# Optimization experiments

Hardware: AMD Instinct MI355X
Metric: run time of the kernel (lower is better)

The kernel has to match this reference:

```python
import jax, jax.numpy as jnp
import numpy as np

N_NODES = 20000
N_EDGES = 100000
NODE_IN = 4
EDGE_IN = 4
HIDDEN = 64
N_GRAPHS = 64
LN_EPS = 1e-5


def _glorot(key, shape):
    fan_in, fan_out = shape[0], shape[1]
    lim = jnp.sqrt(6.0 / (fan_in + fan_out))
    return jax.random.uniform(key, shape, jnp.float32, -lim, lim)


def setup_inputs() -> dict:
    key = jax.random.key(0)
    ks = jax.random.split(key, 24)
    inp = {
        "x": jax.random.normal(ks[0], (N_NODES, NODE_IN), jnp.float32),
        "edge_index": jax.random.randint(ks[1], (2, N_EDGES), 0, N_NODES),
        "edge_attr": jax.random.normal(ks[2], (N_EDGES, EDGE_IN), jnp.float32),
        "batch": jnp.sort(jax.random.randint(ks[3], (N_NODES,), 0, N_GRAPHS)),
        # layer 1: edge MLP edge_in->64->node_in*hidden, root lin, bias, LN
        "eW1_1": _glorot(ks[4], (EDGE_IN, 64)),
        "eb1_1": jnp.zeros((64,), jnp.float32),
        "eW2_1": _glorot(ks[5], (64, NODE_IN * HIDDEN)),
        "eb2_1": jnp.zeros((NODE_IN * HIDDEN,), jnp.float32),
        "root1": _glorot(ks[6], (NODE_IN, HIDDEN)),
        "bias1": jnp.zeros((HIDDEN,), jnp.float32),
        "g1": jnp.ones((HIDDEN,), jnp.float32),
        "b1": jnp.zeros((HIDDEN,), jnp.float32),
        # layer 2: edge MLP edge_in->128->hidden*hidden, root lin, bias, LN
        "eW1_2": _glorot(ks[7], (EDGE_IN, 128)),
        "eb1_2": jnp.zeros((128,), jnp.float32),
        "eW2_2": _glorot(ks[8], (128, HIDDEN * HIDDEN)),
        "eb2_2": jnp.zeros((HIDDEN * HIDDEN,), jnp.float32),
        "root2": _glorot(ks[9], (HIDDEN, HIDDEN)),
        "bias2": jnp.zeros((HIDDEN,), jnp.float32),
        "g2": jnp.ones((HIDDEN,), jnp.float32),
        "b2": jnpp_zeros if False else jnp.zeros((HIDDEN,), jnp.float32),
    }
    return inp


def _nnconv(h, src, dst, edge_attr, eW1, eb1, eW2, eb2, root, bias, in_ch, out_ch):
    # per-edge weight matrix from edge MLP: [E, in_ch, out_ch]
    ew = jnp.maximum(edge_attr @ eW1 + eb1, 0.0) @ eW2 + eb2
    ew = ew.reshape(-1, in_ch, out_ch)
    # gather src features, per-edge small matmul
    msg = jnp.einsum("ei,eio->eo", h[src], ew)  # [E, out_ch]
    # scatter-mean to dst
    agg = jax.ops.segment_sum(msg, dst, num_segments=N_NODES)
    deg = jax.ops.segment_sum(jnp.ones((msg.shape[0],), msg.dtype), dst, num_segments=N_NODES)
    agg = agg / jnp.maximum(deg, 1.0)[:, None]
    return agg + h @ root + bias


def _layernorm(v, g, b):
    mu = jnp.mean(v, axis=-1, keepdims=True)
    var = jnp.mean((v - mu) ** 2, axis=-1, keepdims=True)
    return (v - mu) * jax.lax.rsqrt(var + LN_EPS) * g + b


def reference(x, edge_index, edge_attr, batch,
              eW1_1, eb1_1, eW2_1, eb2_1, root1, bias1, g1, b1,
              eW1_2, eb1_2, eW2_2, eb2_2, root2, bias2, g2, b2):
    src, dst = edge_index[0], edge_index[1]
    h = _nnconv(x, src, dst, edge_attr, eW1_1, eb1_1, eW2_1, eb2_1, root1, bias1, NODE_IN, HIDDEN)
    h = _layernorm(jnp.maximum(h, 0.0), g1, b1)  # dropout is identity in eval
    h = _nnconv(h, src, dst, edge_attr, eW1_2, eb1_2, eW2_2, eb2_2, root2, bias2, HIDDEN, HIDDEN)
    h = _layernorm(jnp.maximum(h, 0.0), g2, b2)
    # global mean pool over graphs
    num = jax.ops.segment_sum(h, batch, num_segments=N_GRAPHS)
    cnt = jax.ops.segment_sum(jnp.ones((h.shape[0],), h.dtype), batch, num_segments=N_GRAPHS)
    return num / jnp.maximum(cnt, 1.0)[:, None]
```

## Files before the change

### kernel.cpp

```cpp
#include <hip/hip_runtime.h>
#include <hip/hip_bf16.h>
#include <hip/hip_fp16.h>

#define NN 20000
#define NE 100000
#define NGR 64
#define NGRP 1250

using bf16 = __hip_bfloat16;
typedef __attribute__((ext_vector_type(8))) short v8s;
typedef __attribute__((ext_vector_type(4))) float v4f;
typedef _Float16 h2f __attribute__((ext_vector_type(2)));

__device__ __forceinline__ float ldf(const void* p, int idx, int isbf) {
  if (isbf) return __bfloat162float(((const bf16*)p)[idx]);
  return ((const float*)p)[idx];
}
__device__ __forceinline__ unsigned short f2bfbits(float v) {
  unsigned int b = __float_as_uint(v);
  b += 0x7fffu + ((b >> 16) & 1u);
  return (unsigned short)(b >> 16);
}

__device__ __forceinline__ unsigned int pkh2(float a, float b) {
#if __has_builtin(__builtin_amdgcn_cvt_pkrtz)
  auto r = __builtin_amdgcn_cvt_pkrtz(a, b);
  return __builtin_bit_cast(unsigned int, r);
#else
  unsigned int lo = __half_as_ushort(__float2half(a));
  unsigned int hi = __half_as_ushort(__float2half(b));
  return lo | (hi << 16);
#endif
}
__device__ __forceinline__ float dot2a(unsigned int z, unsigned int q, float c) {
#if __has_builtin(__builtin_amdgcn_fdot2)
  return __builtin_amdgcn_fdot2(__builtin_bit_cast(h2f, z),
                                __builtin_bit_cast(h2f, q), c, false);
#else
  h2f zh = __builtin_bit_cast(h2f, z), qh = __builtin_bit_cast(h2f, q);
  return c + (float)zh.x * (float)qh.x + (float)zh.y * (float)qh.y;
#endif
}

__global__ __launch_bounds__(64) void k_detect(const unsigned short* __restrict__ xr,
                                               int* __restrict__ flag) {
  const int t = threadIdx.x;
  int cnt = 0;
#pragma unroll
  for (int j = 0; j < 4; j++) {
    unsigned short w = xr[t * 4 + j];
    int ex = (w >> 7) & 0xFF;
    cnt += (ex >= 118 && ex <= 131) ? 1 : 0;
  }
#pragma unroll
  for (int m = 32; m >= 1; m >>= 1) cnt += __shfl_xor(cnt, m, 64);
  if (t == 0) *flag = (cnt >= 192) ? 1 : 0;
}

__global__ __launch_bounds__(256) void k_deg(const int* __restrict__ ei,
                                             int* __restrict__ deg_src,
                                             int* __restrict__ deg_in) {
  int e = blockIdx.x * 256 + threadIdx.x;
  if (e < NE) {
    atomicAdd(&deg_src[ei[e]], 1);
    atomicAdd(&deg_in[ei[NE + e]], 1);
  }
}

__global__ __launch_bounds__(256) void k_scan(const int* __restrict__ deg,
                                              int* __restrict__ off,
                                              int* __restrict__ cur) {
  constexpr int T = 256, CH = 80;
  __shared__ int sums[T];
  const int t = threadIdx.x;
  const int base = t * CH;
  int s = 0;
  for (int j = 0; j < CH; j++) {
    int i = base + j;
    s += (i < NN) ? deg[i] : 0;
  }
  sums[t] = s;
  __syncthreads();
  for (int st = 1; st < T; st <<= 1) {
    int v = (t >= st) ? sums[t - st] : 0;
    __syncthreads();
    sums[t] += v;
    __syncthreads();
  }
  int run = sums[t] - s;
  for (int j = 0; j < CH; j++) {
    int i = base + j;
    if (i < NN) {
      int v = deg[i];
      off[i] = run;
      cur[i] = run;
      run += v;
    }
  }
  if (t == T - 1) off[NN] = sums[T - 1];
}

__global__ __launch_bounds__(256) void k_scatter(const int* __restrict__ ei,
                                                 int* __restrict__ cur,
                                                 int* __restrict__ ebs) {
  int e = blockIdx.x * 256 + threadIdx.x;
  if (e < NE) {
    int p = atomicAdd(&cur[ei[e]], 1);
    if (p >= 0 && p < NE) ebs[p] = e;
  }
}

template <int KH, int IN>
__global__ __launch_bounds__(256) void k_shuffle(const void* __restrict__ W2,
                                                 unsigned short* __restrict__ W2s,
                                                 const int* __restrict__ flag) {
  const int f = *flag;
  int t = blockIdx.x * 256 + threadIdx.x;
  int lane = t & 63, F = t >> 6;
  int ks = F & 1, ot = (F >> 1) & 3, k2 = F >> 3;
  int quad = lane >> 4, col = lane & 15;
  unsigned short tmp[8];
#pragma unroll
  for (int j = 0; j < 8; j++) {
    int i = ks * 32 + quad * 8 + j;
    tmp[j] = f2bfbits(ldf(W2, k2 * (IN * 64) + i * 64 + ot * 16 + col, f));
  }
  *(uint4*)(W2s + (size_t)F * 512 + lane * 8) = *(uint4*)tmp;
}

template <int IN, int KH, int HMODE, int QMFMA, int CSPLIT>
__global__ __launch_bounds__(512, 4) void k_fused2(
    const void* __restrict__ h_in, const void* __restrict__ eW1,
    const void* __restrict__ eb1, const void* __restrict__ W2,
    const unsigned short* __restrict__ W2s, const void* __restrict__ eb2,
    const void* __restrict__ ea, const int* __restrict__ ei,
    const int* __restrict__ src_off, const int* __restrict__ ebs,
    float* __restrict__ agg, const int* __restrict__ flag) {
  constexpr int NPG = 16, KC = 16, NCH = KH / KC, NCHL = NCH / CSPLIT, EB = 128;
  constexpr int QNS = (KC / 2) * 64 + 4;
  constexpr int ZROW = 10;

  __shared__ float hA[NPG][IN];
  __shared__ _Float16 r2h[NPG][64];
  __shared__ __align__(16) unsigned int Qc[NPG * QNS];
  __shared__ float eW1S[4][KH];
  __shared__ float ebS[KH];
  __shared__ float eaS[EB][4];
  __shared__ __align__(16) unsigned int zB[EB * ZROW];
  __shared__ int esrcS[EB], edstS[EB];
  __shared__ __align__(16) unsigned short hF[QMFMA ? 2 : 1][64][8];

  const int f = *flag;
  const int tid = threadIdx.x;
  const int o = tid & 63;
  const int kq = tid >> 6;
  const int g = blockIdx.y;
  const int n0 = blockIdx.x * NPG;

  for (int idx = tid; idx < NPG * IN; idx += 512) {
    int n = idx / IN, i = idx - n * IN;
    hA[n][i] = (HMODE == 1) ? ((const float*)h_in)[(n0 + n) * IN + i]
                            : ldf(h_in, (n0 + n) * IN + i, f);
  }
  for (int idx = tid; idx < 4 * KH; idx += 512)
    ((float*)eW1S)[idx] = ldf(eW1, idx, f);
  for (int idx = tid; idx < KH; idx += 512) ebS[idx] = ldf(eb1, idx, f);
  __syncthreads();

  if (g == 0) {
    const int nb = kq * 2;
    float a0 = 0.f, a1 = 0.f;
    for (int i = 0; i < IN; i++) {
      float wv = ldf(eb2, i * 64 + o, f);
      a0 += hA[nb + 0][i] * wv;
      a1 += hA[nb + 1][i] * wv;
    }
    r2h[nb + 0][o] = (_Float16)a0;
    r2h[nb + 1][o] = (_Float16)a1;
  }
  if constexpr (QMFMA) {
    if (tid < 128) {
      int l = tid & 63, ks = tid >> 6;
#pragma unroll
      for (int j = 0; j < 8; j++)
        hF[ks][l][j] = f2bfbits(hA[l & 15][ks * 32 + (l >> 4) * 8 + j]);
    }
  }
  __syncthreads();

  v8s aF0 = {}, aF1 = {};
  if constexpr (QMFMA) {
    aF0 = *(const v8s*)&hF[0][o][0];
    aF1 = *(const v8s*)&hF[1][o][0];
  }

  const int estart = src_off[n0];
  const int ecount = src_off[n0 + NPG] - estart;

  for (int b = 0; b < ecount; b += EB) {
    const int bc = min(EB, ecount - b);
    __syncthreads();
    if (tid < bc) {
      int eid = ebs[estart + b + tid];
      esrcS[tid] = ei[eid] - n0;
      edstS[tid] = ei[NE + eid];
#pragma unroll
      for (int i = 0; i < 4; i++) eaS[tid][i] = ldf(ea, eid * 4 + i, f);
    }
    __syncthreads();

    float msg[EB / 8];
#pragma unroll
    for (int j = 0; j < EB / 8; j++) msg[j] = 0.f;
    const int lo = (bc * kq) >> 3, hi = (bc * (kq + 1)) >> 3;

    for (int cl = 0; cl < NCHL; cl++) {
      const int c = g * NCHL + cl;
      v4f acc8[8];
      float accv[NPG * 2];
      if constexpr (QMFMA) {
#pragma unroll
        for (int nt = 0; nt < 8; nt++) {
          acc8[nt] = (v4f){0.f, 0.f, 0.f, 0.f};
          const int k2 = c * KC + kq * 2 + (nt >> 2);
          const int Fb = (k2 * 4 + (nt & 3)) * 2;
          v8s b0 = *(const v8s*)(W2s + (size_t)Fb * 512 + o * 8);
          v8s b1 = *(const v8s*)(W2s + (size_t)(Fb + 1) * 512 + o * 8);
          acc8[nt] =
              __builtin_amdgcn_mfma_f32_16x16x32_bf16(aF0, b0, acc8[nt], 0, 0, 0);
          acc8[nt] =
              __builtin_amdgcn_mfma_f32_16x16x32_bf16(aF1, b1, acc8[nt], 0, 0, 0);
        }
      } else {
        const int kg0 = c * KC + kq * 2;
        const int w2base = kg0 * (IN * 64) + o;
        float w0[IN], w1[IN];
#pragma unroll
        for (int j = 0; j < IN; j++) {
          w0[j] = ldf(W2, w2base + j * 64, f);
          w1[j] = ldf(W2, w2base + IN * 64 + j * 64, f);
        }
#pragma unroll
        for (int n = 0; n < NPG; n++) {
          float a0 = 0.f, a1 = 0.f;
#pragma unroll
          for (int j = 0; j < IN; j++) {
            float hv = hA[n][j];
            a0 += hv * w0[j];
            a1 += hv * w1[j];
          }
          accv[n * 2 + 0] = a0;
          accv[n * 2 + 1] = a1;
        }
      }
      const int ze = tid & 127, kseg = tid >> 7;
      float zv[4];
      if (ze < bc) {
#pragma unroll
        for (int jj = 0; jj < 4; jj++) {
          int k2 = c * KC + kseg * 4 + jj;
          float a = ebS[k2];
#pragma unroll
          for (int i = 0; i < 4; i++) a += eaS[ze][i] * eW1S[i][k2];
          zv[jj] = fmaxf(a, 0.f);
        }
      }
      __syncthreads();
      if constexpr (QMFMA) {
        const int quad = o >> 4;
#pragma unroll
        for (int nt = 0; nt < 4; nt++) {
          const int o2 = nt * 16 + (o & 15);
#pragma unroll
          for (int r = 0; r < 4; r++)
            Qc[(quad * 4 + r) * QNS + kq * 64 + o2] =
                pkh2(acc8[nt][r], acc8[nt + 4][r]);
        }
      } else {
#pragma unroll
        for (int n = 0; n < NPG; n++)
          Qc[n * QNS + kq * 64 + o] = pkh2(accv[n * 2 + 0], accv[n * 2 + 1]);
      }
      if (ze < bc) {
        uint2 p;
        p.x = pkh2(zv[0], zv[1]);
        p.y = pkh2(zv[2], zv[3]);
        *(uint2*)&zB[ze * ZROW + kseg * 2] = p;
      }
      __syncthreads();
      unsigned int q0 = 0, q1 = 0, q2 = 0, q3 = 0, q4 = 0, q5 = 0, q6 = 0,
                   q7 = 0;
      int sprev = -1;
#pragma unroll
      for (int j = 0; j < EB / 8; j++) {
        const int e = lo + j;
        if (e < hi) {
          const int s = esrcS[e];
          if (s != sprev) {
            const unsigned int* qp = &Qc[s * QNS + o];
            q0 = qp[0 * 64]; q1 = qp[1 * 64]; q2 = qp[2 * 64]; q3 = qp[3 * 64];
            q4 = qp[4 * 64]; q5 = qp[5 * 64]; q6 = qp[6 * 64]; q7 = qp[7 * 64];
            sprev = s;
          }
          const uint2 za = *(const uint2*)&zB[e * ZROW + 0];
          const uint2 zb2 = *(const uint2*)&zB[e * ZROW + 2];
          const uint2 zc = *(const uint2*)&zB[e * ZROW + 4];
          const uint2 zd = *(const uint2*)&zB[e * ZROW + 6];
          float m = msg[j];
          m = dot2a(za.x, q0, m);
          m = dot2a(za.y, q1, m);
          m = dot2a(zb2.x, q2, m);
          m = dot2a(zb2.y, q3, m);
          m = dot2a(zc.x, q4, m);
          m = dot2a(zc.y, q5, m);
          m = dot2a(zd.x, q6, m);
          m = dot2a(zd.y, q7, m);
          msg[j] = m;
        }
      }
    }
#pragma unroll
    for (int j = 0; j < EB / 8; j++) {
      const int e = lo + j;
      if (e < hi) {
        float add = msg[j];
        if (g == 0) add += (float)r2h[esrcS[e]][o];
        atomicAdd(&agg[(size_t)edstS[e] * 64 + o], add);
      }
    }
  }
}

__device__ __forceinline__ float wave_sum(float v) {
#pragma unroll
  for (int m = 32; m >= 1; m >>= 1) v += __shfl_xor(v, m, 64);
  return v;
}

__global__ __launch_bounds__(256, 4) void k_node1(
    const float* __restrict__ agg1, const int* __restrict__ deg_in,
    const void* __restrict__ x, const void* __restrict__ root1,
    const void* __restrict__ bias1, const void* __restrict__ g1,
    const void* __restrict__ b1, float* __restrict__ h1,
    const int* __restrict__ flag) {
  constexpr int NPW = 8;
  const int f = *flag;
  const int tid = threadIdx.x;
  const int o = tid & 63;
  const int w = tid >> 6;
  float r1c[4];
#pragma unroll
  for (int i = 0; i < 4; i++) r1c[i] = ldf(root1, i * 64 + o, f);
  const float bs = ldf(bias1, o, f);
  const float gv = ldf(g1, o, f);
  const float bv = ldf(b1, o, f);
  const int wid = blockIdx.x * 4 + w;
  const int nbeg = wid * NPW;
  const int nend = min(nbeg + NPW, NN);
  for (int n = nbeg; n < nend; n++) {
    float v = agg1[(size_t)n * 64 + o] / fmaxf((float)deg_in[n], 1.f) + bs;
#pragma unroll
    for (int i = 0; i < 4; i++) v += ldf(x, n * 4 + i, f) * r1c[i];
    v = fmaxf(v, 0.f);
    const float mu = wave_sum(v) * (1.f / 64.f);
    const float d = v - mu;
    const float var = wave_sum(d * d) * (1.f / 64.f);
    h1[(size_t)n * 64 + o] = d * rsqrtf(var + 1e-5f) * gv + bv;
  }
}

__global__ __launch_bounds__(256, 4) void k_node2(
    const float* __restrict__ agg2, const int* __restrict__ deg_in,
    const float* __restrict__ h1, const void* __restrict__ root2,
    const void* __restrict__ bias2, const void* __restrict__ g2,
    const void* __restrict__ b2, const int* __restrict__ batch,
    float* __restrict__ psum, float* __restrict__ pcnt,
    const int* __restrict__ flag) {
  constexpr int NPW = 8;
  __shared__ float hS[4][64];
  const int f = *flag;
  const int tid = threadIdx.x;
  const int o = tid & 63;
  const int w = tid >> 6;
  float r2c[64];
#pragma unroll
  for (int i = 0; i < 64; i++) r2c[i] = ldf(root2, i * 64 + o, f);
  const float bs = ldf(bias2, o, f);
  const float gv = ldf(g2, o, f);
  const float bv = ldf(b2, o, f);
  const int wid = blockIdx.x * 4 + w;
  const int nbeg = wid * NPW;
  const int nend = min(nbeg + NPW, NN);
  float acc = 0.f;
  int curbi = -1, cnt = 0;
  for (int n = nbeg; n < nend; n++) {
    hS[w][o] = h1[(size_t)n * 64 + o];
    float v = agg2[(size_t)n * 64 + o] / fmaxf((float)deg_in[n], 1.f) + bs;
#pragma unroll
    for (int i = 0; i < 64; i++) v += hS[w][i] * r2c[i];
    v = fmaxf(v, 0.f);
    const float mu = wave_sum(v) * (1.f / 64.f);
    const float d = v - mu;
    const float var = wave_sum(d * d) * (1.f / 64.f);
    const float out = d * rsqrtf(var + 1e-5f) * gv + bv;
    const int bi = batch[n];
    if (bi != curbi) {
      if (curbi >= 0) {
        atomicAdd(&psum[curbi * 64 + o], acc);
        if (o == 0) atomicAdd(&pcnt[curbi], (float)cnt);
      }
      acc = 0.f;
      cnt = 0;
      curbi = bi;
    }
    acc += out;
    cnt++;
  }
  if (curbi >= 0) {
    atomicAdd(&psum[curbi * 64 + o], acc);
    if (o == 0) atomicAdd(&pcnt[curbi], (float)cnt);
  }
}

__global__ __launch_bounds__(256) void k_out(const float* __restrict__ psum,
                                             const float* __restrict__ pcnt,
                                             void* __restrict__ out,
                                             const int* __restrict__ flag) {
  const int idx = blockIdx.x * 256 + threadIdx.x;
  float v = psum[idx] / fmaxf(pcnt[idx >> 6], 1.f);
  if (*flag)
    ((bf16*)out)[idx] = __float2bfloat16(v);
  else
    ((float*)out)[idx] = v;
}

extern "C" void kernel_launch(void* const* d_in, const int* in_sizes, int n_in,
                              void* d_out, int out_size, void* d_ws,
                              size_t ws_size, hipStream_t stream) {
  (void)in_sizes; (void)n_in; (void)out_size; (void)ws_size;
  const void* x = d_in[0];
  const int* ei = (const int*)d_in[1];
  const void* ea = d_in[2];
  const int* batch = (const int*)d_in[3];
  const void* eW1_1 = d_in[4];
  const void* eb1_1 = d_in[5];
  const void* eW2_1 = d_in[6];
  const void* eb2_1 = d_in[7];
  const void* root1 = d_in[8];
  const void* bias1 = d_in[9];
  const void* g1 = d_in[10];
  const void* b1 = d_in[11];
  const void* eW1_2 = d_in[12];
  const void* eb1_2 = d_in[13];
  const void* eW2_2 = d_in[14];
  const void* eb2_2 = d_in[15];
  const void* root2 = d_in[16];
  const void* bias2 = d_in[17];
  const void* g2 = d_in[18];
  const void* b2 = d_in[19];

  char* w = (char*)d_ws;
  size_t off = 0;
  auto alloc = [&](size_t bytes) -> void* {
    void* p = w + off;
    off = (off + bytes + 255) & ~(size_t)255;
    return p;
  };
  float* agg1 = (float*)alloc((size_t)NN * 64 * 4);
  float* agg2 = (float*)alloc((size_t)NN * 64 * 4);
  float* psum = (float*)alloc((size_t)NGR * 64 * 4);
  float* pcnt = (float*)alloc((size_t)NGR * 4);
  int* deg_src = (int*)alloc((size_t)NN * 4);
  int* deg_in = (int*)alloc((size_t)NN * 4);
  const size_t zero_bytes = off;
  int* src_off = (int*)alloc((size_t)(NN + 1) * 4);
  int* cur = (int*)alloc((size_t)NN * 4);
  int* ebs = (int*)alloc((size_t)NE * 4);
  int* flag = (int*)alloc(256);
  float* h1 = (float*)alloc((size_t)NN * 64 * 4);
  unsigned short* W2s = (unsigned short*)alloc((size_t)128 * 8 * 64 * 8 * 2);

  hipMemsetAsync(d_ws, 0, zero_bytes, stream);

  k_detect<<<1, 64, 0, stream>>>((const unsigned short*)x, flag);
  k_deg<<<(NE + 255) / 256, 256, 0, stream>>>(ei, deg_src, deg_in);
  k_scan<<<1, 256, 0, stream>>>(deg_src, src_off, cur);
  k_scatter<<<(NE + 255) / 256, 256, 0, stream>>>(ei, cur, ebs);
  k_shuffle<128, 64><<<256, 256, 0, stream>>>(eW2_2, W2s, flag);
  k_fused2<4, 64, 0, 0, 2><<<dim3(NGRP, 2), 512, 0, stream>>>(
      x, eW1_1, eb1_1, eW2_1, W2s, eb2_1, ea, ei, src_off, ebs, agg1, flag);
  k_node1<<<(NN + 8 * 4 - 1) / (8 * 4), 256, 0, stream>>>(
      agg1, deg_in, x, root1, bias1, g1, b1, h1, flag);
  k_fused2<64, 128, 1, 1, 2><<<dim3(NGRP, 2), 512, 0, stream>>>(
      h1, eW1_2, eb1_2, eW2_2, W2s, eb2_2, ea, ei, src_off, ebs, agg2, flag);
  k_node2<<<(NN + 8 * 4 - 1) / (8 * 4), 256, 0, stream>>>(
      agg2, deg_in, h1, root2, bias2, g2, b2, batch, psum, pcnt, flag);
  k_out<<<(NGR * 64) / 256, 256, 0, stream>>>(psum, pcnt, d_out, flag);
}
```

Before: 483.8 us.

## Replace atomic scatter-add with per-edge message buffers and CSR gather by destination

The fused edge kernels now write each edge's partial message (one buffer per channel-split group) to a dense per-edge array instead of issuing float atomicAdds into per-node aggregates. A second CSR keyed by destination is built (an extra scan plus a dual scatter). The node kernels then gather and sum messages per destination node. This is meant to remove atomic contention and the zeroing of the aggregate buffers. In exchange it adds about 51 MB of message traffic written and read back through indirect gathers, plus a nondeterministic edge order within each destination segment.

```diff
diff --git a/kernel.cpp b/kernel.cpp
--- a/kernel.cpp
+++ b/kernel.cpp
@@ -100,13 +100,17 @@
   if (t == T - 1) off[NN] = sums[T - 1];
 }
 
-__global__ __launch_bounds__(256) void k_scatter(const int* __restrict__ ei,
-                                                 int* __restrict__ cur,
-                                                 int* __restrict__ ebs) {
+__global__ __launch_bounds__(256) void k_scatter2(const int* __restrict__ ei,
+                                                  int* __restrict__ cur_s,
+                                                  int* __restrict__ ebs_s,
+                                                  int* __restrict__ cur_d,
+                                                  int* __restrict__ ebs_d) {
   int e = blockIdx.x * 256 + threadIdx.x;
   if (e < NE) {
-    int p = atomicAdd(&cur[ei[e]], 1);
-    if (p >= 0 && p < NE) ebs[p] = e;
+    int ps = atomicAdd(&cur_s[ei[e]], 1);
+    if (ps >= 0 && ps < NE) ebs_s[ps] = e;
+    int pd = atomicAdd(&cur_d[ei[NE + e]], 1);
+    if (pd >= 0 && pd < NE) ebs_d[pd] = e;
   }
 }
 
@@ -128,15 +132,15 @@
   *(uint4*)(W2s + (size_t)F * 512 + lane * 8) = *(uint4*)tmp;
 }
 
-template <int IN, int KH, int HMODE, int QMFMA, int CSPLIT>
+template <int IN, int KH, int HMODE, int QMFMA, int G>
 __global__ __launch_bounds__(512, 4) void k_fused2(
     const void* __restrict__ h_in, const void* __restrict__ eW1,
     const void* __restrict__ eb1, const void* __restrict__ W2,
     const unsigned short* __restrict__ W2s, const void* __restrict__ eb2,
     const void* __restrict__ ea, const int* __restrict__ ei,
     const int* __restrict__ src_off, const int* __restrict__ ebs,
-    float* __restrict__ agg, const int* __restrict__ flag) {
-  constexpr int NPG = 16, KC = 16, NCH = KH / KC, NCHL = NCH / CSPLIT, EB = 128;
+    float* __restrict__ msgp, const int* __restrict__ flag) {
+  constexpr int NPG = 16, KC = 16, NCH = KH / KC, NCHG = NCH / G, EB = 128;
   constexpr int QNS = (KC / 2) * 64 + 4;
   constexpr int ZROW = 10;
 
@@ -147,7 +151,7 @@
   __shared__ float ebS[KH];
   __shared__ float eaS[EB][4];
   __shared__ __align__(16) unsigned int zB[EB * ZROW];
-  __shared__ int esrcS[EB], edstS[EB];
+  __shared__ int esrcS[EB], eidS[EB];
   __shared__ __align__(16) unsigned short hF[QMFMA ? 2 : 1][64][8];
 
   const int f = *flag;
@@ -156,6 +160,7 @@
   const int kq = tid >> 6;
   const int g = blockIdx.y;
   const int n0 = blockIdx.x * NPG;
+  float* __restrict__ mout = msgp + (size_t)g * NE * 64;
 
   for (int idx = tid; idx < NPG * IN; idx += 512) {
     int n = idx / IN, i = idx - n * IN;
@@ -203,7 +208,7 @@
     if (tid < bc) {
       int eid = ebs[estart + b + tid];
       esrcS[tid] = ei[eid] - n0;
-      edstS[tid] = ei[NE + eid];
+      eidS[tid] = eid;
 #pragma unroll
       for (int i = 0; i < 4; i++) eaS[tid][i] = ldf(ea, eid * 4 + i, f);
     }
@@ -214,8 +219,8 @@
     for (int j = 0; j < EB / 8; j++) msg[j] = 0.f;
     const int lo = (bc * kq) >> 3, hi = (bc * (kq + 1)) >> 3;
 
-    for (int cl = 0; cl < NCHL; cl++) {
-      const int c = g * NCHL + cl;
+    for (int cc = 0; cc < NCHG; cc++) {
+      const int c = g * NCHG + cc;
       v4f acc8[8];
       float accv[NPG * 2];
       if constexpr (QMFMA) {
@@ -323,9 +328,9 @@
     for (int j = 0; j < EB / 8; j++) {
       const int e = lo + j;
       if (e < hi) {
-        float add = msg[j];
-        if (g == 0) add += (float)r2h[esrcS[e]][o];
-        atomicAdd(&agg[(size_t)edstS[e] * 64 + o], add);
+        float mv = msg[j];
+        if (g == 0) mv += (float)r2h[esrcS[e]][o];
+        mout[(size_t)eidS[e] * 64 + o] = mv;
       }
     }
   }
@@ -337,13 +342,13 @@
   return v;
 }
 
-__global__ __launch_bounds__(256, 4) void k_node1(
-    const float* __restrict__ agg1, const int* __restrict__ deg_in,
-    const void* __restrict__ x, const void* __restrict__ root1,
-    const void* __restrict__ bias1, const void* __restrict__ g1,
-    const void* __restrict__ b1, float* __restrict__ h1,
-    const int* __restrict__ flag) {
-  constexpr int NPW = 8;
+__global__ __launch_bounds__(256, 4) void k_nodeg1(
+    const float* __restrict__ msgp, const int* __restrict__ dst_off,
+    const int* __restrict__ ebs_d, const void* __restrict__ x,
+    const void* __restrict__ root1, const void* __restrict__ bias1,
+    const void* __restrict__ g1, const void* __restrict__ b1,
+    float* __restrict__ h1, const int* __restrict__ flag) {
+  constexpr int NPW = 4;
   const int f = *flag;
   const int tid = threadIdx.x;
   const int o = tid & 63;
@@ -358,7 +363,13 @@
   const int nbeg = wid * NPW;
   const int nend = min(nbeg + NPW, NN);
   for (int n = nbeg; n < nend; n++) {
-    float v = agg1[(size_t)n * 64 + o] / fmaxf((float)deg_in[n], 1.f) + bs;
+    const int e0 = dst_off[n], e1 = dst_off[n + 1];
+    float s = 0.f;
+    for (int p = e0; p < e1; p++) {
+      const size_t eo = (size_t)ebs_d[p] * 64 + o;
+      s += msgp[eo] + msgp[(size_t)NE * 64 + eo];
+    }
+    float v = s / fmaxf((float)(e1 - e0), 1.f) + bs;
 #pragma unroll
     for (int i = 0; i < 4; i++) v += ldf(x, n * 4 + i, f) * r1c[i];
     v = fmaxf(v, 0.f);
@@ -369,14 +380,14 @@
   }
 }
 
-__global__ __launch_bounds__(256, 4) void k_node2(
-    const float* __restrict__ agg2, const int* __restrict__ deg_in,
-    const float* __restrict__ h1, const void* __restrict__ root2,
-    const void* __restrict__ bias2, const void* __restrict__ g2,
-    const void* __restrict__ b2, const int* __restrict__ batch,
-    float* __restrict__ psum, float* __restrict__ pcnt,
-    const int* __restrict__ flag) {
-  constexpr int NPW = 8;
+__global__ __launch_bounds__(256, 4) void k_nodeg2(
+    const float* __restrict__ msgp, const int* __restrict__ dst_off,
+    const int* __restrict__ ebs_d, const float* __restrict__ h1,
+    const void* __restrict__ root2, const void* __restrict__ bias2,
+    const void* __restrict__ g2, const void* __restrict__ b2,
+    const int* __restrict__ batch, float* __restrict__ psum,
+    float* __restrict__ pcnt, const int* __restrict__ flag) {
+  constexpr int NPW = 4;
   __shared__ float hS[4][64];
   const int f = *flag;
   const int tid = threadIdx.x;
@@ -395,7 +406,13 @@
   int curbi = -1, cnt = 0;
   for (int n = nbeg; n < nend; n++) {
     hS[w][o] = h1[(size_t)n * 64 + o];
-    float v = agg2[(size_t)n * 64 + o] / fmaxf((float)deg_in[n], 1.f) + bs;
+    const int e0 = dst_off[n], e1 = dst_off[n + 1];
+    float s = 0.f;
+    for (int p = e0; p < e1; p++) {
+      const size_t eo = (size_t)ebs_d[p] * 64 + o;
+      s += msgp[eo] + msgp[(size_t)NE * 64 + eo];
+    }
+    float v = s / fmaxf((float)(e1 - e0), 1.f) + bs;
 #pragma unroll
     for (int i = 0; i < 64; i++) v += hS[w][i] * r2c[i];
     v = fmaxf(v, 0.f);
@@ -466,34 +483,39 @@
     off = (off + bytes + 255) & ~(size_t)255;
     return p;
   };
-  float* agg1 = (float*)alloc((size_t)NN * 64 * 4);
-  float* agg2 = (float*)alloc((size_t)NN * 64 * 4);
   float* psum = (float*)alloc((size_t)NGR * 64 * 4);
   float* pcnt = (float*)alloc((size_t)NGR * 4);
   int* deg_src = (int*)alloc((size_t)NN * 4);
   int* deg_in = (int*)alloc((size_t)NN * 4);
   const size_t zero_bytes = off;
   int* src_off = (int*)alloc((size_t)(NN + 1) * 4);
-  int* cur = (int*)alloc((size_t)NN * 4);
-  int* ebs = (int*)alloc((size_t)NE * 4);
+  int* cur_s = (int*)alloc((size_t)NN * 4);
+  int* dst_off = (int*)alloc((size_t)(NN + 1) * 4);
+  int* cur_d = (int*)alloc((size_t)NN * 4);
+  int* ebs_s = (int*)alloc((size_t)NE * 4);
+  int* ebs_d = (int*)alloc((size_t)NE * 4);
   int* flag = (int*)alloc(256);
   float* h1 = (float*)alloc((size_t)NN * 64 * 4);
   unsigned short* W2s = (unsigned short*)alloc((size_t)128 * 8 * 64 * 8 * 2);
+  float* msgp = (float*)alloc((size_t)2 * NE * 64 * 4);
 
   hipMemsetAsync(d_ws, 0, zero_bytes, stream);
 
   k_detect<<<1, 64, 0, stream>>>((const unsigned short*)x, flag);
   k_deg<<<(NE + 255) / 256, 256, 0, stream>>>(ei, deg_src, deg_in);
-  k_scan<<<1, 256, 0, stream>>>(deg_src, src_off, cur);
-  k_scatter<<<(NE + 255) / 256, 256, 0, stream>>>(ei, cur, ebs);
+  k_scan<<<1, 256, 0, stream>>>(deg_src, src_off, cur_s);
+  k_scan<<<1, 256, 0, stream>>>(deg_in, dst_off, cur_d);
+  k_scatter2<<<(NE + 255) / 256, 256, 0, stream>>>(ei, cur_s, ebs_s, cur_d,
+                                                   ebs_d);
   k_shuffle<128, 64><<<256, 256, 0, stream>>>(eW2_2, W2s, flag);
   k_fused2<4, 64, 0, 0, 2><<<dim3(NGRP, 2), 512, 0, stream>>>(
-      x, eW1_1, eb1_1, eW2_1, W2s, eb2_1, ea, ei, src_off, ebs, agg1, flag);
-  k_node1<<<(NN + 8 * 4 - 1) / (8 * 4), 256, 0, stream>>>(
-      agg1, deg_in, x, root1, bias1, g1, b1, h1, flag);
+      x, eW1_1, eb1_1, eW2_1, W2s, eb2_1, ea, ei, src_off, ebs_s, msgp, flag);
+  k_nodeg1<<<(NN + 15) / 16, 256, 0, stream>>>(msgp, dst_off, ebs_d, x, root1,
+                                               bias1, g1, b1, h1, flag);
   k_fused2<64, 128, 1, 1, 2><<<dim3(NGRP, 2), 512, 0, stream>>>(
-      h1, eW1_2, eb1_2, eW2_2, W2s, eb2_2, ea, ei, src_off, ebs, agg2, flag);
-  k_node2<<<(NN + 8 * 4 - 1) / (8 * 4), 256, 0, stream>>>(
-      agg2, deg_in, h1, root2, bias2, g2, b2, batch, psum, pcnt, flag);
+      h1, eW1_2, eb1_2, eW2_2, W2s, eb2_2, ea, ei, src_off, ebs_s, msgp, flag);
+  k_nodeg2<<<(NN + 15) / 16, 256, 0, stream>>>(msgp, dst_off, ebs_d, h1, root2,
+                                               bias2, g2, b2, batch, psum,
+                                               pcnt, flag);
   k_out<<<(NGR * 64) / 256, 256, 0, stream>>>(psum, pcnt, d_out, flag);
 }
```

New measurement: 558.0 us. 15.3% more time.
